# Kernel tuning notes

Hardware: AMD Instinct MI355X
Metric: run time of the kernel (lower is better)

The kernel has to match this reference:

```python
import jax, jax.numpy as jnp
import numpy as np

N_EMBD = 1024
N_HEAD = 16
HEAD = N_EMBD // N_HEAD
B, T = 4, 2048


def setup_inputs() -> dict:
    key = jax.random.key(0)
    ks = jax.random.split(key, 9)
    s = 1.0 / np.sqrt(N_EMBD)
    return {
        "x": jax.random.normal(ks[0], (B, T, N_EMBD), dtype=jnp.float32),
        "Wk": jax.random.uniform(ks[1], (N_EMBD, N_EMBD), jnp.float32, -s, s),
        "bk": jax.random.uniform(ks[2], (N_EMBD,), jnp.float32, -s, s),
        "Wq": jax.random.uniform(ks[3], (N_EMBD, N_EMBD), jnp.float32, -s, s),
        "bq": jax.random.uniform(ks[4], (N_EMBD,), jnp.float32, -s, s),
        "Wv": jax.random.uniform(ks[5], (N_EMBD, N_EMBD), jnp.float32, -s, s),
        "bv": jax.random.uniform(ks[6], (N_EMBD,), jnp.float32, -s, s),
        "Wp": jax.random.uniform(ks[7], (N_EMBD, N_EMBD), jnp.float32, -s, s),
        "bp": jax.random.uniform(ks[8], (N_EMBD,), jnp.float32, -s, s),
    }


def reference(x, Wk, bk, Wq, bq, Wv, bv, Wp, bp):
    b, t, c = x.shape
    # torch Linear: y = x @ W.T + b
    def heads(W, bias):
        return (x @ W.T + bias).reshape(b, t, N_HEAD, HEAD).transpose(0, 2, 1, 3)
    k = heads(Wk, bk)  # [B,H,T,D]
    q = heads(Wq, bq)
    v = heads(Wv, bv)
    att = jnp.einsum("bhqd,bhkd->bhqk", q, k) * (1.0 / np.sqrt(HEAD))
    causal = jnp.tril(jnp.ones((t, t), dtype=bool))
    att = jnp.where(causal, att, -jnp.inf)
    att = jax.nn.softmax(att, axis=-1)
    y = jnp.einsum("bhqk,bhkd->bhqd", att, v)  # [B,H,T,D]
    y = y.transpose(0, 2, 1, 3).reshape(b, t, c)
    return y @ Wp.T + bp
```

## Files before the change

kernel.cpp:

```cpp
#include <hip/hip_runtime.h>
#include <stdint.h>

typedef short bf16x8 __attribute__((ext_vector_type(8)));
typedef float f32x4 __attribute__((ext_vector_type(4)));
typedef float f32x16 __attribute__((ext_vector_type(16)));

#define MFMA16(a, b, c) __builtin_amdgcn_mfma_f32_16x16x32_bf16((a), (b), (c), 0, 0, 0)
#define MFMA32(a, b, c) __builtin_amdgcn_mfma_f32_32x32x16_bf16((a), (b), (c), 0, 0, 0)

__device__ __forceinline__ unsigned short f2bf(float x) {
  union { float f; unsigned int u; } v; v.f = x;
  unsigned int r = (v.u + 0x7FFFu + ((v.u >> 16) & 1u)) >> 16;
  return (unsigned short)r;
}

__device__ __forceinline__ unsigned int cvtpk(float lo, float hi) {
  unsigned int r;
  asm("v_cvt_pk_bf16_f32 %0, %1, %2" : "=v"(r) : "v"(lo), "v"(hi));
  return r;
}

__device__ __forceinline__ void plswap(unsigned int& a, unsigned int& b) {
  asm("v_permlane32_swap_b32 %0, %1" : "+v"(a), "+v"(b));
}

__device__ __forceinline__ float exp2f_fast(float x) {
  float r;
  asm("v_exp_f32 %0, %1" : "=v"(r) : "v"(x));
  return r;
}

__global__ void __launch_bounds__(256) cvt_all(const float* __restrict__ x,
                                               const float* __restrict__ Wk,
                                               const float* __restrict__ Wq,
                                               const float* __restrict__ Wv,
                                               const float* __restrict__ Wp,
                                               unsigned short* __restrict__ xb,
                                               unsigned short* __restrict__ wqkvb,
                                               unsigned short* __restrict__ wpb) {
  const int stride = gridDim.x * blockDim.x;
  for (int i = blockIdx.x * blockDim.x + threadIdx.x; i < 3145728; i += stride) {
    if (i < 2097152) {
      float4 v = ((const float4*)x)[i];
      ushort4 o;
      o.x = f2bf(v.x); o.y = f2bf(v.y); o.z = f2bf(v.z); o.w = f2bf(v.w);
      ((ushort4*)xb)[i] = o;
      continue;
    }
    int j = i - 2097152;
    int sec = j >> 18;
    int off = j & 262143;
    const float4* s4 = (const float4*)(sec == 0 ? Wk : sec == 1 ? Wq : sec == 2 ? Wv : Wp);
    float4 v = s4[off];
    ushort4 o;
    o.x = f2bf(v.x); o.y = f2bf(v.y); o.z = f2bf(v.z); o.w = f2bf(v.w);
    if (sec < 3) ((ushort4*)wqkvb)[j] = o;
    else ((ushort4*)wpb)[off] = o;
  }
}

template <int MODE, int NX, int CPX>
__global__ void __launch_bounds__(512) gemm_big(const unsigned short* __restrict__ A,
                                                const unsigned short* __restrict__ Bw,
                                                const float* __restrict__ b0,
                                                const float* __restrict__ b1,
                                                const float* __restrict__ b2,
                                                unsigned short* __restrict__ O0,
                                                unsigned short* __restrict__ O1,
                                                unsigned short* __restrict__ O2,
                                                float* __restrict__ Of) {
  extern __shared__ unsigned short lds[];

  const int tid = threadIdx.x;
  const int wid = tid >> 6;
  const int l = tid & 63;
  const int g = l >> 4;
  const int ln = l & 15;

  const int bid = blockIdx.x;
  const int swz = (bid & 7) * CPX + (bid >> 3);
  const int bx = swz % NX;
  const int by = swz / NX;
  const int m0 = by * 256;
  const int n0 = bx * 128;
  const int wm = (wid >> 1) * 64;
  const int wn = (wid & 1) * 64;

  f32x4 acc[4][4];
#pragma unroll
  for (int i = 0; i < 4; ++i)
#pragma unroll
    for (int j = 0; j < 4; ++j) acc[i][j] = (f32x4){0.f, 0.f, 0.f, 0.f};

#define STAGE_G(bufi, kt)                                                                         \
  {                                                                                               \
    unsigned short* Ad = lds + (bufi)*16384;                                                      \
    unsigned short* Bd = lds + 32768 + (bufi)*8192;                                               \
    _Pragma("unroll") for (int i = 0; i < 4; ++i) {                                               \
      int c = i * 512 + tid;                                                                      \
      int row = c >> 3;                                                                           \
      int cs = (c & 7) ^ (row & 7);                                                               \
      const unsigned short* ga = A + (size_t)(m0 + row) * 1024 + (kt) + cs * 8;                   \
      __builtin_amdgcn_global_load_lds((const __attribute__((address_space(1))) void*)ga,         \
                                       (__attribute__((address_space(3))) void*)&Ad[c * 8],       \
                                       16, 0, 0);                                                 \
    }                                                                                             \
    _Pragma("unroll") for (int i = 0; i < 2; ++i) {                                               \
      int c = i * 512 + tid;                                                                      \
      int row = c >> 3;                                                                           \
      int cs = (c & 7) ^ (row & 7);                                                               \
      const unsigned short* gb = Bw + (size_t)(n0 + row) * 1024 + (kt) + cs * 8;                  \
      __builtin_amdgcn_global_load_lds((const __attribute__((address_space(1))) void*)gb,         \
                                       (__attribute__((address_space(3))) void*)&Bd[c * 8],       \
                                       16, 0, 0);                                                 \
    }                                                                                             \
  }

  STAGE_G(0, 0);
  __syncthreads();

  for (int T = 0; T < 16; ++T) {
    const int buf = T & 1;
    if (T < 15) STAGE_G(buf ^ 1, (T + 1) * 64);

    const unsigned short* Ar = lds + buf * 16384;
    const unsigned short* Br = lds + 32768 + buf * 8192;
#pragma unroll
    for (int kk = 0; kk < 2; ++kk) {
      bf16x8 af[4], bfr[4];
#pragma unroll
      for (int mi = 0; mi < 4; ++mi) {
        int ra = wm + mi * 16 + ln;
        af[mi] = *(const bf16x8*)&Ar[ra * 64 + (((kk << 2) + g) ^ (ra & 7)) * 8];
      }
#pragma unroll
      for (int ni = 0; ni < 4; ++ni) {
        int rb = wn + ni * 16 + ln;
        bfr[ni] = *(const bf16x8*)&Br[rb * 64 + (((kk << 2) + g) ^ (rb & 7)) * 8];
      }
      __builtin_amdgcn_s_setprio(1);
#pragma unroll
      for (int mi = 0; mi < 4; ++mi)
#pragma unroll
        for (int ni = 0; ni < 4; ++ni) acc[mi][ni] = MFMA16(af[mi], bfr[ni], acc[mi][ni]);
      __builtin_amdgcn_s_setprio(0);
    }
    __syncthreads();
  }
#undef STAGE_G

  const int mBase = m0 + wm + g * 4;
  const int nBase = n0 + wn + ln;

  if (MODE == 1) {
#pragma unroll
    for (int mi = 0; mi < 4; ++mi) {
      int mg = mBase + mi * 16;
#pragma unroll
      for (int ni = 0; ni < 4; ++ni) {
        int n = nBase + ni * 16;
        float bvl = b0[n];
#pragma unroll
        for (int r = 0; r < 4; ++r) Of[(size_t)(mg + r) * 1024 + n] = acc[mi][ni][r] + bvl;
      }
    }
  } else {
    const int sec = n0 >> 10;
    const float* bias = (sec == 0) ? b0 : (sec == 1) ? b1 : b2;
#pragma unroll
    for (int mi = 0; mi < 4; ++mi) {
      int mg = mBase + mi * 16;
      int b = mg >> 11, t = mg & 2047;
#pragma unroll
      for (int ni = 0; ni < 4; ++ni) {
        int n = nBase + ni * 16;
        int nn = n & 1023;
        int h = nn >> 6, d = nn & 63;
        float bvl = bias[nn];
        if (sec == 2) {
          ushort4 pk;
          pk.x = f2bf(acc[mi][ni][0] + bvl);
          pk.y = f2bf(acc[mi][ni][1] + bvl);
          pk.z = f2bf(acc[mi][ni][2] + bvl);
          pk.w = f2bf(acc[mi][ni][3] + bvl);
          *(ushort4*)&O2[((size_t)((b * 16 + h) * 64 + d)) * 2048 + t] = pk;
        } else {
          unsigned short* O = sec ? O1 : O0;
          const float sc = sec ? (0.125f * 1.44269504f) : 1.0f;
#pragma unroll
          for (int r = 0; r < 4; ++r)
            O[((size_t)(b * 16 + h) * 2048 + (t + r)) * 64 + d] = f2bf((acc[mi][ni][r] + bvl) * sc);
        }
      }
    }
  }
}

__global__ void __launch_bounds__(512) attn_kernel(const unsigned short* __restrict__ Q,
                                                   const unsigned short* __restrict__ K,
                                                   const unsigned short* __restrict__ Vt,
                                                   unsigned short* __restrict__ Y) {
  __shared__ unsigned short Ks[2][64 * 64];
  __shared__ unsigned short Vs[2][64 * 64];

  const int tid = threadIdx.x;
  const int wid = tid >> 6;
  const int l = tid & 63;
  const int q32 = l & 31;
  const int hi = l >> 5;
  const int bh = blockIdx.x & 63;
  const int u = blockIdx.x >> 6;
  const int j = (u < 4) ? u : (11 - u);
  const int qblk = (wid < 4) ? (15 - j) : j;
  const int q0w = qblk * 128 + (wid & 3) * 32;
  const int NT = 2 * (15 - j) + 2;
  const int myNt = (q0w + 95) >> 6;

  const unsigned short* Qp = Q + (size_t)bh * 2048 * 64;
  const unsigned short* Kp = K + (size_t)bh * 2048 * 64;
  const unsigned short* Vp = Vt + (size_t)bh * 64 * 2048;
  const int b = bh >> 4, h = bh & 15;

  const int srow = tid >> 3;
  const int csw = (tid & 7) ^ (srow & 7);

  bf16x8 qf[4];
#pragma unroll
  for (int kk = 0; kk < 4; ++kk)
    qf[kk] = *(const bf16x8*)&Qp[(size_t)(q0w + q32) * 64 + kk * 16 + hi * 8];

  f32x16 o0, o1;
#pragma unroll
  for (int r = 0; r < 16; ++r) { o0[r] = 0.f; o1[r] = 0.f; }
  float m = -1e30f, lst = 0.f;

#define STAGE(bufi, kk0)                                                                        \
  {                                                                                             \
    const unsigned short* gk = Kp + (size_t)((kk0) + srow) * 64 + csw * 8;                      \
    const unsigned short* gv = Vp + (size_t)srow * 2048 + (kk0) + csw * 8;                      \
    __builtin_amdgcn_global_load_lds((const __attribute__((address_space(1))) void*)gk,         \
                                     (__attribute__((address_space(3))) void*)                  \
                                         &Ks[bufi][wid * 512],                                  \
                                     16, 0, 0);                                                 \
    __builtin_amdgcn_global_load_lds((const __attribute__((address_space(1))) void*)gv,         \
                                     (__attribute__((address_space(3))) void*)                  \
                                         &Vs[bufi][wid * 512],                                  \
                                     16, 0, 0);                                                 \
  }

  int buf = 0;
  STAGE(0, 0);
  __syncthreads();

  for (int t = 0; t < NT; ++t) {
    const int k0 = t * 64;
    if (t + 1 < NT) STAGE(buf ^ 1, k0 + 64);

    if (t < myNt) {
      const int xr = q32 & 7;
      f32x16 s0, s1;
#pragma unroll
      for (int r = 0; r < 16; ++r) { s0[r] = 0.f; s1[r] = 0.f; }
      __builtin_amdgcn_s_setprio(1);
#pragma unroll
      for (int kk = 0; kk < 4; ++kk) {
        bf16x8 kf0 = *(const bf16x8*)&Ks[buf][q32 * 64 + (((kk << 1) | hi) ^ xr) * 8];
        bf16x8 kf1 = *(const bf16x8*)&Ks[buf][(32 + q32) * 64 + (((kk << 1) | hi) ^ xr) * 8];
        s0 = MFMA32(kf0, qf[kk], s0);
        s1 = MFMA32(kf1, qf[kk], s1);
      }
      __builtin_amdgcn_s_setprio(0);

      if (k0 + 63 > q0w) {
        const int qg = q0w + q32;
#pragma unroll
        for (int r = 0; r < 16; ++r) {
          int kr = (r & 3) + 8 * (r >> 2) + 4 * hi;
          if (k0 + kr > qg) s0[r] = -1e30f;
          if (k0 + 32 + kr > qg) s1[r] = -1e30f;
        }
      }

      float pm = fmaxf(fmaxf(s0[0], s0[1]), s0[2]);
#pragma unroll
      for (int r = 3; r < 15; r += 3) pm = fmaxf(fmaxf(fmaxf(s0[r], s0[r + 1]), s0[r + 2]), pm);
      pm = fmaxf(pm, s0[15]);
#pragma unroll
      for (int r = 0; r < 15; r += 3) pm = fmaxf(fmaxf(fmaxf(s1[r], s1[r + 1]), s1[r + 2]), pm);
      pm = fmaxf(pm, s1[15]);
      pm = fmaxf(pm, __shfl_xor(pm, 32));

      if (__any(pm > m + 11.0f)) {
        float mn = fmaxf(m, pm);
        float sf = exp2f_fast(m - mn);
        m = mn;
        lst *= sf;
#pragma unroll
        for (int r = 0; r < 16; ++r) {
          float sb2 = __shfl(sf, (r & 3) + 8 * (r >> 2) + 4 * hi);
          o0[r] *= sb2;
          o1[r] *= sb2;
        }
      }
      float rs = 0.f;
#pragma unroll
      for (int r = 0; r < 16; ++r) { s0[r] = exp2f_fast(s0[r] - m); rs += s0[r]; }
#pragma unroll
      for (int r = 0; r < 16; ++r) { s1[r] = exp2f_fast(s1[r] - m); rs += s1[r]; }
      rs += __shfl_xor(rs, 32);
      lst += rs;

      union { unsigned int u[4]; bf16x8 v; } pa[4];
#pragma unroll
      for (int t2 = 0; t2 < 2; ++t2) {
        const f32x16& sv = t2 ? s1 : s0;
#pragma unroll
        for (int sl = 0; sl < 2; ++sl) {
          int base = sl * 8;
          unsigned int x0 = cvtpk(sv[base + 0], sv[base + 1]);
          unsigned int x1 = cvtpk(sv[base + 2], sv[base + 3]);
          unsigned int x2 = cvtpk(sv[base + 4], sv[base + 5]);
          unsigned int x3 = cvtpk(sv[base + 6], sv[base + 7]);
          plswap(x0, x2);
          plswap(x1, x3);
          int ksg = t2 * 2 + sl;
          pa[ksg].u[0] = x0; pa[ksg].u[1] = x1; pa[ksg].u[2] = x2; pa[ksg].u[3] = x3;
        }
      }

      __builtin_amdgcn_s_setprio(1);
#pragma unroll
      for (int ksg = 0; ksg < 4; ++ksg) {
        bf16x8 v0 = *(const bf16x8*)&Vs[buf][q32 * 64 + (((ksg << 1) | hi) ^ xr) * 8];
        bf16x8 v1 = *(const bf16x8*)&Vs[buf][(32 + q32) * 64 + (((ksg << 1) | hi) ^ xr) * 8];
        o0 = MFMA32(pa[ksg].v, v0, o0);
        o1 = MFMA32(pa[ksg].v, v1, o1);
      }
      __builtin_amdgcn_s_setprio(0);
    }

    __syncthreads();
    buf ^= 1;
  }

#pragma unroll
  for (int r = 0; r < 16; ++r) {
    int qsrc = (r & 3) + 8 * (r >> 2) + 4 * hi;
    int qg = q0w + qsrc;
    float lq = __shfl(lst, qsrc);
    float inv = 1.0f / lq;
    size_t rowb = (size_t)(b * 2048 + qg) * 1024 + h * 64;
    Y[rowb + q32] = f2bf(o0[r] * inv);
    Y[rowb + 32 + q32] = f2bf(o1[r] * inv);
  }
#undef STAGE
}

extern "C" void kernel_launch(void* const* d_in, const int* in_sizes, int n_in,
                              void* d_out, int out_size, void* d_ws, size_t ws_size,
                              hipStream_t stream) {
  const float* x = (const float*)d_in[0];
  const float* Wk = (const float*)d_in[1];
  const float* bk = (const float*)d_in[2];
  const float* Wq = (const float*)d_in[3];
  const float* bq = (const float*)d_in[4];
  const float* Wv = (const float*)d_in[5];
  const float* bv = (const float*)d_in[6];
  const float* Wp = (const float*)d_in[7];
  const float* bp = (const float*)d_in[8];
  float* out = (float*)d_out;

  char* ws = (char*)d_ws;
  unsigned short* xb    = (unsigned short*)(ws);
  unsigned short* wqkvb = (unsigned short*)(ws + 16777216);
  unsigned short* wpb   = (unsigned short*)(ws + 23068672);
  unsigned short* Qb    = (unsigned short*)(ws + 25165824);
  unsigned short* Kb    = (unsigned short*)(ws + 41943040);
  unsigned short* Vtb   = (unsigned short*)(ws + 58720256);
  unsigned short* yb    = (unsigned short*)(ws + 75497472);
  if (ws_size < 92274688u) return;

  const int LDS_BYTES = 98304;
  (void)hipFuncSetAttribute((const void*)&gemm_big<0, 24, 96>,
                            hipFuncAttributeMaxDynamicSharedMemorySize, LDS_BYTES);
  (void)hipFuncSetAttribute((const void*)&gemm_big<1, 8, 32>,
                            hipFuncAttributeMaxDynamicSharedMemorySize, LDS_BYTES);

  cvt_all<<<dim3(3072), dim3(256), 0, stream>>>(x, Wk, Wq, Wv, Wp, xb, wqkvb, wpb);

  gemm_big<0, 24, 96><<<dim3(768), dim3(512), LDS_BYTES, stream>>>(
      xb, wqkvb, bk, bq, bv, Kb, Qb, Vtb, nullptr);

  attn_kernel<<<dim3(512), dim3(512), 0, stream>>>(Qb, Kb, Vtb, yb);

  gemm_big<1, 8, 32><<<dim3(256), dim3(512), LDS_BYTES, stream>>>(
      yb, wpb, bp, nullptr, nullptr, nullptr, nullptr, nullptr, out);
}
```

Before: 152.2 us.

## Process two query chunks per wave in attention to reuse staged K/V tiles

Each attention workgroup now handles two 128-row query chunks per wave (a late and an early chunk paired for causal balance) and halves the grid to 256 blocks. Every staged K/V tile in LDS is used by both chunks, which halves global K/V traffic and barrier count per unit of work. The cost is doubled accumulator and Q-fragment registers, which may lower occupancy or cause spills. Fewer blocks also means less parallelism across CUs.

```diff
diff --git a/kernel.cpp b/kernel.cpp
--- a/kernel.cpp
+++ b/kernel.cpp
@@ -196,6 +196,93 @@
   }
 }
 
+__device__ __forceinline__ void attn_tile(const unsigned short* __restrict__ Kbuf,
+                                          const unsigned short* __restrict__ Vbuf,
+                                          const bf16x8* qf, f32x16& o0, f32x16& o1,
+                                          float& m, float& lst, int k0, int q0w,
+                                          int q32, int hi) {
+  const int xr = q32 & 7;
+  f32x16 s0, s1;
+#pragma unroll
+  for (int r = 0; r < 16; ++r) { s0[r] = 0.f; s1[r] = 0.f; }
+  __builtin_amdgcn_s_setprio(1);
+#pragma unroll
+  for (int kk = 0; kk < 4; ++kk) {
+    bf16x8 kf0 = *(const bf16x8*)&Kbuf[q32 * 64 + (((kk << 1) | hi) ^ xr) * 8];
+    bf16x8 kf1 = *(const bf16x8*)&Kbuf[(32 + q32) * 64 + (((kk << 1) | hi) ^ xr) * 8];
+    s0 = MFMA32(kf0, qf[kk], s0);
+    s1 = MFMA32(kf1, qf[kk], s1);
+  }
+  __builtin_amdgcn_s_setprio(0);
+
+  if (k0 + 63 > q0w) {
+    const int qg = q0w + q32;
+#pragma unroll
+    for (int r = 0; r < 16; ++r) {
+      int kr = (r & 3) + 8 * (r >> 2) + 4 * hi;
+      if (k0 + kr > qg) s0[r] = -1e30f;
+      if (k0 + 32 + kr > qg) s1[r] = -1e30f;
+    }
+  }
+
+  float pm = fmaxf(fmaxf(s0[0], s0[1]), s0[2]);
+#pragma unroll
+  for (int r = 3; r < 15; r += 3) pm = fmaxf(fmaxf(fmaxf(s0[r], s0[r + 1]), s0[r + 2]), pm);
+  pm = fmaxf(pm, s0[15]);
+#pragma unroll
+  for (int r = 0; r < 15; r += 3) pm = fmaxf(fmaxf(fmaxf(s1[r], s1[r + 1]), s1[r + 2]), pm);
+  pm = fmaxf(pm, s1[15]);
+  pm = fmaxf(pm, __shfl_xor(pm, 32));
+
+  if (__any(pm > m + 11.0f)) {
+    float mn = fmaxf(m, pm);
+    float sf = exp2f_fast(m - mn);
+    m = mn;
+    lst *= sf;
+#pragma unroll
+    for (int r = 0; r < 16; ++r) {
+      float sb2 = __shfl(sf, (r & 3) + 8 * (r >> 2) + 4 * hi);
+      o0[r] *= sb2;
+      o1[r] *= sb2;
+    }
+  }
+  float rs = 0.f;
+#pragma unroll
+  for (int r = 0; r < 16; ++r) { s0[r] = exp2f_fast(s0[r] - m); rs += s0[r]; }
+#pragma unroll
+  for (int r = 0; r < 16; ++r) { s1[r] = exp2f_fast(s1[r] - m); rs += s1[r]; }
+  rs += __shfl_xor(rs, 32);
+  lst += rs;
+
+  union { unsigned int u[4]; bf16x8 v; } pa[4];
+#pragma unroll
+  for (int t2 = 0; t2 < 2; ++t2) {
+    const f32x16& sv = t2 ? s1 : s0;
+#pragma unroll
+    for (int sl = 0; sl < 2; ++sl) {
+      int base = sl * 8;
+      unsigned int x0 = cvtpk(sv[base + 0], sv[base + 1]);
+      unsigned int x1 = cvtpk(sv[base + 2], sv[base + 3]);
+      unsigned int x2 = cvtpk(sv[base + 4], sv[base + 5]);
+      unsigned int x3 = cvtpk(sv[base + 6], sv[base + 7]);
+      plswap(x0, x2);
+      plswap(x1, x3);
+      int ksg = t2 * 2 + sl;
+      pa[ksg].u[0] = x0; pa[ksg].u[1] = x1; pa[ksg].u[2] = x2; pa[ksg].u[3] = x3;
+    }
+  }
+
+  __builtin_amdgcn_s_setprio(1);
+#pragma unroll
+  for (int ksg = 0; ksg < 4; ++ksg) {
+    bf16x8 v0 = *(const bf16x8*)&Vbuf[q32 * 64 + (((ksg << 1) | hi) ^ xr) * 8];
+    bf16x8 v1 = *(const bf16x8*)&Vbuf[(32 + q32) * 64 + (((ksg << 1) | hi) ^ xr) * 8];
+    o0 = MFMA32(pa[ksg].v, v0, o0);
+    o1 = MFMA32(pa[ksg].v, v1, o1);
+  }
+  __builtin_amdgcn_s_setprio(0);
+}
+
 __global__ void __launch_bounds__(512) attn_kernel(const unsigned short* __restrict__ Q,
                                                    const unsigned short* __restrict__ K,
                                                    const unsigned short* __restrict__ Vt,
@@ -210,11 +297,15 @@
   const int hi = l >> 5;
   const int bh = blockIdx.x & 63;
   const int u = blockIdx.x >> 6;
-  const int j = (u < 4) ? u : (11 - u);
-  const int qblk = (wid < 4) ? (15 - j) : j;
-  const int q0w = qblk * 128 + (wid & 3) * 32;
-  const int NT = 2 * (15 - j) + 2;
-  const int myNt = (q0w + 95) >> 6;
+  const int wl = wid & 3;
+
+  const int chA = (wid < 4) ? (15 - u) : (8 + u);
+  const int chB = (wid < 4) ? u : (7 - u);
+  const int qA0 = chA * 128 + wl * 32;
+  const int qB0 = chB * 128 + wl * 32;
+  const int NT = 2 * (15 - u) + 2;
+  const int myNtA = (qA0 + 95) >> 6;
+  const int myNtB = (qB0 + 95) >> 6;
 
   const unsigned short* Qp = Q + (size_t)bh * 2048 * 64;
   const unsigned short* Kp = K + (size_t)bh * 2048 * 64;
@@ -224,15 +315,17 @@
   const int srow = tid >> 3;
   const int csw = (tid & 7) ^ (srow & 7);
 
-  bf16x8 qf[4];
-#pragma unroll
-  for (int kk = 0; kk < 4; ++kk)
-    qf[kk] = *(const bf16x8*)&Qp[(size_t)(q0w + q32) * 64 + kk * 16 + hi * 8];
-
-  f32x16 o0, o1;
-#pragma unroll
-  for (int r = 0; r < 16; ++r) { o0[r] = 0.f; o1[r] = 0.f; }
-  float m = -1e30f, lst = 0.f;
+  bf16x8 qfA[4], qfB[4];
+#pragma unroll
+  for (int kk = 0; kk < 4; ++kk) {
+    qfA[kk] = *(const bf16x8*)&Qp[(size_t)(qA0 + q32) * 64 + kk * 16 + hi * 8];
+    qfB[kk] = *(const bf16x8*)&Qp[(size_t)(qB0 + q32) * 64 + kk * 16 + hi * 8];
+  }
+
+  f32x16 o0A, o1A, o0B, o1B;
+#pragma unroll
+  for (int r = 0; r < 16; ++r) { o0A[r] = 0.f; o1A[r] = 0.f; o0B[r] = 0.f; o1B[r] = 0.f; }
+  float mA = -1e30f, lstA = 0.f, mB = -1e30f, lstB = 0.f;
 
 #define STAGE(bufi, kk0)                                                                        \
   {                                                                                             \
@@ -256,88 +349,8 @@
     const int k0 = t * 64;
     if (t + 1 < NT) STAGE(buf ^ 1, k0 + 64);
 
-    if (t < myNt) {
-      const int xr = q32 & 7;
-      f32x16 s0, s1;
-#pragma unroll
-      for (int r = 0; r < 16; ++r) { s0[r] = 0.f; s1[r] = 0.f; }
-      __builtin_amdgcn_s_setprio(1);
-#pragma unroll
-      for (int kk = 0; kk < 4; ++kk) {
-        bf16x8 kf0 = *(const bf16x8*)&Ks[buf][q32 * 64 + (((kk << 1) | hi) ^ xr) * 8];
-        bf16x8 kf1 = *(const bf16x8*)&Ks[buf][(32 + q32) * 64 + (((kk << 1) | hi) ^ xr) * 8];
-        s0 = MFMA32(kf0, qf[kk], s0);
-        s1 = MFMA32(kf1, qf[kk], s1);
-      }
-      __builtin_amdgcn_s_setprio(0);
-
-      if (k0 + 63 > q0w) {
-        const int qg = q0w + q32;
-#pragma unroll
-        for (int r = 0; r < 16; ++r) {
-          int kr = (r & 3) + 8 * (r >> 2) + 4 * hi;
-          if (k0 + kr > qg) s0[r] = -1e30f;
-          if (k0 + 32 + kr > qg) s1[r] = -1e30f;
-        }
-      }
-
-      float pm = fmaxf(fmaxf(s0[0], s0[1]), s0[2]);
-#pragma unroll
-      for (int r = 3; r < 15; r += 3) pm = fmaxf(fmaxf(fmaxf(s0[r], s0[r + 1]), s0[r + 2]), pm);
-      pm = fmaxf(pm, s0[15]);
-#pragma unroll
-      for (int r = 0; r < 15; r += 3) pm = fmaxf(fmaxf(fmaxf(s1[r], s1[r + 1]), s1[r + 2]), pm);
-      pm = fmaxf(pm, s1[15]);
-      pm = fmaxf(pm, __shfl_xor(pm, 32));
-
-      if (__any(pm > m + 11.0f)) {
-        float mn = fmaxf(m, pm);
-        float sf = exp2f_fast(m - mn);
-        m = mn;
-        lst *= sf;
-#pragma unroll
-        for (int r = 0; r < 16; ++r) {
-          float sb2 = __shfl(sf, (r & 3) + 8 * (r >> 2) + 4 * hi);
-          o0[r] *= sb2;
-          o1[r] *= sb2;
-        }
-      }
-      float rs = 0.f;
-#pragma unroll
-      for (int r = 0; r < 16; ++r) { s0[r] = exp2f_fast(s0[r] - m); rs += s0[r]; }
-#pragma unroll
-      for (int r = 0; r < 16; ++r) { s1[r] = exp2f_fast(s1[r] - m); rs += s1[r]; }
-      rs += __shfl_xor(rs, 32);
-      lst += rs;
-
-      union { unsigned int u[4]; bf16x8 v; } pa[4];
-#pragma unroll
-      for (int t2 = 0; t2 < 2; ++t2) {
-        const f32x16& sv = t2 ? s1 : s0;
-#pragma unroll
-        for (int sl = 0; sl < 2; ++sl) {
-          int base = sl * 8;
-          unsigned int x0 = cvtpk(sv[base + 0], sv[base + 1]);
-          unsigned int x1 = cvtpk(sv[base + 2], sv[base + 3]);
-          unsigned int x2 = cvtpk(sv[base + 4], sv[base + 5]);
-          unsigned int x3 = cvtpk(sv[base + 6], sv[base + 7]);
-          plswap(x0, x2);
-          plswap(x1, x3);
-          int ksg = t2 * 2 + sl;
-          pa[ksg].u[0] = x0; pa[ksg].u[1] = x1; pa[ksg].u[2] = x2; pa[ksg].u[3] = x3;
-        }
-      }
-
-      __builtin_amdgcn_s_setprio(1);
-#pragma unroll
-      for (int ksg = 0; ksg < 4; ++ksg) {
-        bf16x8 v0 = *(const bf16x8*)&Vs[buf][q32 * 64 + (((ksg << 1) | hi) ^ xr) * 8];
-        bf16x8 v1 = *(const bf16x8*)&Vs[buf][(32 + q32) * 64 + (((ksg << 1) | hi) ^ xr) * 8];
-        o0 = MFMA32(pa[ksg].v, v0, o0);
-        o1 = MFMA32(pa[ksg].v, v1, o1);
-      }
-      __builtin_amdgcn_s_setprio(0);
-    }
+    if (t < myNtA) attn_tile(Ks[buf], Vs[buf], qfA, o0A, o1A, mA, lstA, k0, qA0, q32, hi);
+    if (t < myNtB) attn_tile(Ks[buf], Vs[buf], qfB, o0B, o1B, mB, lstB, k0, qB0, q32, hi);
 
     __syncthreads();
     buf ^= 1;
@@ -346,12 +359,16 @@
 #pragma unroll
   for (int r = 0; r < 16; ++r) {
     int qsrc = (r & 3) + 8 * (r >> 2) + 4 * hi;
-    int qg = q0w + qsrc;
-    float lq = __shfl(lst, qsrc);
-    float inv = 1.0f / lq;
-    size_t rowb = (size_t)(b * 2048 + qg) * 1024 + h * 64;
-    Y[rowb + q32] = f2bf(o0[r] * inv);
-    Y[rowb + 32 + q32] = f2bf(o1[r] * inv);
+    float lqA = __shfl(lstA, qsrc);
+    float lqB = __shfl(lstB, qsrc);
+    float invA = 1.0f / lqA;
+    float invB = 1.0f / lqB;
+    size_t rowA = (size_t)(b * 2048 + qA0 + qsrc) * 1024 + h * 64;
+    size_t rowB = (size_t)(b * 2048 + qB0 + qsrc) * 1024 + h * 64;
+    Y[rowA + q32] = f2bf(o0A[r] * invA);
+    Y[rowA + 32 + q32] = f2bf(o1A[r] * invA);
+    Y[rowB + q32] = f2bf(o0B[r] * invB);
+    Y[rowB + 32 + q32] = f2bf(o1B[r] * invB);
   }
 #undef STAGE
 }
@@ -391,7 +408,7 @@
   gemm_big<0, 24, 96><<<dim3(768), dim3(512), LDS_BYTES, stream>>>(
       xb, wqkvb, bk, bq, bv, Kb, Qb, Vtb, nullptr);
 
-  attn_kernel<<<dim3(512), dim3(512), 0, stream>>>(Qb, Kb, Vtb, yb);
+  attn_kernel<<<dim3(256), dim3(512), 0, stream>>>(Qb, Kb, Vtb, yb);
 
   gemm_big<1, 8, 32><<<dim3(256), dim3(512), LDS_BYTES, stream>>>(
       yb, wpb, bp, nullptr, nullptr, nullptr, nullptr, nullptr, out);
```

Result: slower. 163.4 us (+7.4%).

## Add dedicated 256x256-tile QKV GEMM with phased double-buffered LDS pipeline

Applied to the files above, without the earlier changes.

Replaces the templated 256x128 QKV projection GEMM with a dedicated kernel using 256x256 output tiles (each of 8 warps computes 128x64). Loads go straight into LDS through global_load_lds, double-buffered in 64-wide k steps, and each k step is split into four phases that interleave prefetch, barriers and MFMA groups. The larger tile halves the block count and raises arithmetic intensity per LDS byte. In exchange it needs 128KB of LDS and more accumulator registers per thread, and the number of blocks per CU drops. The output-projection GEMM is simplified to its single mode.

```diff
diff --git a/kernel.cpp b/kernel.cpp
--- a/kernel.cpp
+++ b/kernel.cpp
@@ -59,15 +59,147 @@
   }
 }
 
+__global__ void __launch_bounds__(512) gemm_qkv8(const unsigned short* __restrict__ A,
+                                                 const unsigned short* __restrict__ Bw,
+                                                 const float* __restrict__ b0,
+                                                 const float* __restrict__ b1,
+                                                 const float* __restrict__ b2,
+                                                 unsigned short* __restrict__ O0,
+                                                 unsigned short* __restrict__ O1,
+                                                 unsigned short* __restrict__ O2) {
+  extern __shared__ unsigned short lds[];
+#define HBASE(buf, isB, kk) (lds + (buf)*32768 + (isB)*16384 + (kk)*8192)
+
+  const int tid = threadIdx.x;
+  const int wid = tid >> 6;
+  const int l = tid & 63;
+  const int g = l >> 4;
+  const int ln = l & 15;
+
+  const int bid = blockIdx.x;
+  const int swz = (bid & 7) * 48 + (bid >> 3);
+  const int bx = swz % 12;
+  const int by = swz / 12;
+  const int m0 = by * 256;
+  const int n0 = bx * 256;
+  const int wm = (wid >> 2) * 128;
+  const int wn = (wid & 3) * 64;
+
+  f32x4 acc[8][4];
+#pragma unroll
+  for (int i = 0; i < 8; ++i)
+#pragma unroll
+    for (int j = 0; j < 4; ++j) acc[i][j] = (f32x4){0.f, 0.f, 0.f, 0.f};
+
+#define STAGEH(buf, isB, kk, kt)                                                                  \
+  {                                                                                               \
+    unsigned short* dst = HBASE(buf, isB, kk);                                                    \
+    const unsigned short* srcp = (isB) ? Bw : A;                                                  \
+    const int row0 = (isB) ? n0 : m0;                                                             \
+    _Pragma("unroll") for (int i = 0; i < 2; ++i) {                                               \
+      int c = i * 512 + tid;                                                                      \
+      int r = c >> 2;                                                                             \
+      int x = (c & 3) ^ ((r >> 1) & 3);                                                           \
+      const unsigned short* gp = srcp + (size_t)(row0 + r) * 1024 + (kt) + (kk)*32 + x * 8;       \
+      __builtin_amdgcn_global_load_lds((const __attribute__((address_space(1))) void*)gp,         \
+                                       (__attribute__((address_space(3))) void*)&dst[c * 8],      \
+                                       16, 0, 0);                                                 \
+    }                                                                                             \
+  }
+
+  STAGEH(0, 0, 0, 0);
+  STAGEH(0, 1, 0, 0);
+  STAGEH(0, 0, 1, 0);
+  STAGEH(0, 1, 1, 0);
+
+  for (int T = 0; T < 16; ++T) {
+    const int buf = T & 1;
+    const int last = (T == 15);
+    bf16x8 bF[4];
+#pragma unroll
+    for (int ph = 0; ph < 4; ++ph) {
+      const int kk = ph >> 1;
+      const int mg = ph & 1;
+
+      if (mg == 0) {
+        if (!last) asm volatile("s_waitcnt vmcnt(4)" ::: "memory");
+        else asm volatile("s_waitcnt vmcnt(0)" ::: "memory");
+      }
+      if (!last) {
+        if (ph == 0) STAGEH(buf ^ 1, 0, 0, (T + 1) * 64);
+        if (ph == 1) STAGEH(buf ^ 1, 1, 0, (T + 1) * 64);
+        if (ph == 2) STAGEH(buf ^ 1, 0, 1, (T + 1) * 64);
+        if (ph == 3) STAGEH(buf ^ 1, 1, 1, (T + 1) * 64);
+      }
+      if (mg == 0) {
+        __builtin_amdgcn_sched_barrier(0);
+        __builtin_amdgcn_s_barrier();
+        __builtin_amdgcn_sched_barrier(0);
+#pragma unroll
+        for (int ni = 0; ni < 4; ++ni) {
+          int rb = wn + ni * 16 + ln;
+          bF[ni] = *(const bf16x8*)&HBASE(buf, 1, kk)[rb * 32 + (g ^ ((rb >> 1) & 3)) * 8];
+        }
+      }
+      bf16x8 aF[4];
+#pragma unroll
+      for (int j = 0; j < 4; ++j) {
+        int ra = wm + (mg * 4 + j) * 16 + ln;
+        aF[j] = *(const bf16x8*)&HBASE(buf, 0, kk)[ra * 32 + (g ^ ((ra >> 1) & 3)) * 8];
+      }
+      __builtin_amdgcn_s_setprio(1);
+#pragma unroll
+      for (int j = 0; j < 4; ++j)
+#pragma unroll
+        for (int ni = 0; ni < 4; ++ni)
+          acc[mg * 4 + j][ni] = MFMA16(aF[j], bF[ni], acc[mg * 4 + j][ni]);
+      __builtin_amdgcn_s_setprio(0);
+      if (ph == 3) {
+        __builtin_amdgcn_sched_barrier(0);
+        __builtin_amdgcn_s_barrier();
+        __builtin_amdgcn_sched_barrier(0);
+      }
+    }
+  }
+#undef STAGEH
+#undef HBASE
+
+  const int sec = n0 >> 10;
+  const float* bias = (sec == 0) ? b0 : (sec == 1) ? b1 : b2;
+  const int mBase = m0 + wm + g * 4;
+  const int nBase = n0 + wn + ln;
+#pragma unroll
+  for (int mi = 0; mi < 8; ++mi) {
+    int mg2 = mBase + mi * 16;
+    int b = mg2 >> 11, t = mg2 & 2047;
+#pragma unroll
+    for (int ni = 0; ni < 4; ++ni) {
+      int n = nBase + ni * 16;
+      int nn = n & 1023;
+      int h = nn >> 6, d = nn & 63;
+      float bvl = bias[nn];
+      if (sec == 2) {
+        ushort4 pk;
+        pk.x = f2bf(acc[mi][ni][0] + bvl);
+        pk.y = f2bf(acc[mi][ni][1] + bvl);
+        pk.z = f2bf(acc[mi][ni][2] + bvl);
+        pk.w = f2bf(acc[mi][ni][3] + bvl);
+        *(ushort4*)&O2[((size_t)((b * 16 + h) * 64 + d)) * 2048 + t] = pk;
+      } else {
+        unsigned short* O = sec ? O1 : O0;
+        const float sc = sec ? (0.125f * 1.44269504f) : 1.0f;
+#pragma unroll
+        for (int r = 0; r < 4; ++r)
+          O[((size_t)(b * 16 + h) * 2048 + (t + r)) * 64 + d] = f2bf((acc[mi][ni][r] + bvl) * sc);
+      }
+    }
+  }
+}
+
 template <int MODE, int NX, int CPX>
 __global__ void __launch_bounds__(512) gemm_big(const unsigned short* __restrict__ A,
                                                 const unsigned short* __restrict__ Bw,
                                                 const float* __restrict__ b0,
-                                                const float* __restrict__ b1,
-                                                const float* __restrict__ b2,
-                                                unsigned short* __restrict__ O0,
-                                                unsigned short* __restrict__ O1,
-                                                unsigned short* __restrict__ O2,
                                                 float* __restrict__ Of) {
   extern __shared__ unsigned short lds[];
 
@@ -151,47 +283,15 @@
 
   const int mBase = m0 + wm + g * 4;
   const int nBase = n0 + wn + ln;
-
-  if (MODE == 1) {
-#pragma unroll
-    for (int mi = 0; mi < 4; ++mi) {
-      int mg = mBase + mi * 16;
-#pragma unroll
-      for (int ni = 0; ni < 4; ++ni) {
-        int n = nBase + ni * 16;
-        float bvl = b0[n];
-#pragma unroll
-        for (int r = 0; r < 4; ++r) Of[(size_t)(mg + r) * 1024 + n] = acc[mi][ni][r] + bvl;
-      }
-    }
-  } else {
-    const int sec = n0 >> 10;
-    const float* bias = (sec == 0) ? b0 : (sec == 1) ? b1 : b2;
-#pragma unroll
-    for (int mi = 0; mi < 4; ++mi) {
-      int mg = mBase + mi * 16;
-      int b = mg >> 11, t = mg & 2047;
-#pragma unroll
-      for (int ni = 0; ni < 4; ++ni) {
-        int n = nBase + ni * 16;
-        int nn = n & 1023;
-        int h = nn >> 6, d = nn & 63;
-        float bvl = bias[nn];
-        if (sec == 2) {
-          ushort4 pk;
-          pk.x = f2bf(acc[mi][ni][0] + bvl);
-          pk.y = f2bf(acc[mi][ni][1] + bvl);
-          pk.z = f2bf(acc[mi][ni][2] + bvl);
-          pk.w = f2bf(acc[mi][ni][3] + bvl);
-          *(ushort4*)&O2[((size_t)((b * 16 + h) * 64 + d)) * 2048 + t] = pk;
-        } else {
-          unsigned short* O = sec ? O1 : O0;
-          const float sc = sec ? (0.125f * 1.44269504f) : 1.0f;
-#pragma unroll
-          for (int r = 0; r < 4; ++r)
-            O[((size_t)(b * 16 + h) * 2048 + (t + r)) * 64 + d] = f2bf((acc[mi][ni][r] + bvl) * sc);
-        }
-      }
+#pragma unroll
+  for (int mi = 0; mi < 4; ++mi) {
+    int mg = mBase + mi * 16;
+#pragma unroll
+    for (int ni = 0; ni < 4; ++ni) {
+      int n = nBase + ni * 16;
+      float bvl = b0[n];
+#pragma unroll
+      for (int r = 0; r < 4; ++r) Of[(size_t)(mg + r) * 1024 + n] = acc[mi][ni][r] + bvl;
     }
   }
 }
@@ -380,19 +480,18 @@
   unsigned short* yb    = (unsigned short*)(ws + 75497472);
   if (ws_size < 92274688u) return;
 
-  const int LDS_BYTES = 98304;
-  (void)hipFuncSetAttribute((const void*)&gemm_big<0, 24, 96>,
-                            hipFuncAttributeMaxDynamicSharedMemorySize, LDS_BYTES);
+  const int LDS_Q = 131072;
+  const int LDS_P = 98304;
+  (void)hipFuncSetAttribute((const void*)&gemm_qkv8,
+                            hipFuncAttributeMaxDynamicSharedMemorySize, LDS_Q);
   (void)hipFuncSetAttribute((const void*)&gemm_big<1, 8, 32>,
-                            hipFuncAttributeMaxDynamicSharedMemorySize, LDS_BYTES);
+                            hipFuncAttributeMaxDynamicSharedMemorySize, LDS_P);
 
   cvt_all<<<dim3(3072), dim3(256), 0, stream>>>(x, Wk, Wq, Wv, Wp, xb, wqkvb, wpb);
 
-  gemm_big<0, 24, 96><<<dim3(768), dim3(512), LDS_BYTES, stream>>>(
-      xb, wqkvb, bk, bq, bv, Kb, Qb, Vtb, nullptr);
+  gemm_qkv8<<<dim3(384), dim3(512), LDS_Q, stream>>>(xb, wqkvb, bk, bq, bv, Kb, Qb, Vtb);
 
   attn_kernel<<<dim3(512), dim3(512), 0, stream>>>(Qb, Kb, Vtb, yb);
 
-  gemm_big<1, 8, 32><<<dim3(256), dim3(512), LDS_BYTES, stream>>>(
-      yb, wpb, bp, nullptr, nullptr, nullptr, nullptr, nullptr, out);
-}
+  gemm_big<1, 8, 32><<<dim3(256), dim3(512), LDS_P, stream>>>(yb, wpb, bp, out);
+}
```

Measured after the change: 159.4 us. +4.7%, slower.
